# Optimization experiments

Hardware: AMD Instinct MI355X
Metric: run time of the kernel (lower is better)

Reference implementation:

```python
import jax, jax.numpy as jnp
import numpy as np

N_HEADS = 16

def setup_inputs() -> dict:
    key = jax.random.key(0)
    k1, k2, k3 = jax.random.split(key, 3)
    B, L, D = 2, 2048, 1024
    x = jax.random.normal(k1, (B, L, D), dtype=jnp.float32)
    w_qkv = jax.random.normal(k2, (D, 3 * D), dtype=jnp.float32) * (1.0 / np.sqrt(D))
    w_out = jax.random.normal(k3, (D, D), dtype=jnp.float32) * (1.0 / np.sqrt(D))
    return {"x": x, "w_qkv": w_qkv, "w_out": w_out}

def reference(x, w_qkv, w_out):
    B, L, D = x.shape
    H = N_HEADS
    dh = D // H
    qkv = x @ w_qkv                      # (B, L, 3D)
    q, k, v = jnp.split(qkv, 3, axis=-1)
    # (B, H, L, dh)
    q = q.reshape(B, L, H, dh).transpose(0, 2, 1, 3)
    k = k.reshape(B, L, H, dh).transpose(0, 2, 1, 3)
    v = v.reshape(B, L, H, dh).transpose(0, 2, 1, 3)
    scale = 1.0 / jnp.sqrt(jnp.asarray(dh, x.dtype))
    attn = jnp.einsum('bhqd,bhkd->bhqk', q, k) * scale   # (B, H, L, L)
    causal = jnp.tril(jnp.ones((L, L), dtype=bool))
    attn = jnp.where(causal[None, None], attn, -jnp.inf)
    attn = jax.nn.softmax(attn, axis=-1)
    out = jnp.einsum('bhqk,bhkd->bhqd', attn, v)         # (B, H, L, dh)
    out = out.transpose(0, 2, 1, 3).reshape(B, L, D)
    return out @ w_out
```

## Files before the change

### kernel.cpp

```cpp
#include <hip/hip_runtime.h>

typedef __attribute__((ext_vector_type(4))) float f32x4;
typedef __attribute__((ext_vector_type(16))) float f32x16;
typedef __attribute__((ext_vector_type(8))) __bf16 bf16x8;
typedef __attribute__((ext_vector_type(4))) __bf16 bf16x4;
typedef __attribute__((ext_vector_type(4))) unsigned u32x4;
typedef __attribute__((ext_vector_type(2))) unsigned u32x2;

static __device__ __forceinline__ f32x4 mfma16(bf16x8 a, bf16x8 b, f32x4 c) {
    return __builtin_amdgcn_mfma_f32_16x16x32_bf16(a, b, c, 0, 0, 0);
}
static __device__ __forceinline__ f32x16 mfma32(bf16x8 a, bf16x8 b, f32x16 c) {
    return __builtin_amdgcn_mfma_f32_32x32x16_bf16(a, b, c, 0, 0, 0);
}
static __device__ __forceinline__ unsigned pk_bf16(float a, float b) {
    unsigned lo = __builtin_bit_cast(unsigned short, (__bf16)a);
    unsigned hh = __builtin_bit_cast(unsigned short, (__bf16)b);
    return lo | (hh << 16);
}

#define QSCALE 0.18033688f

__global__ __launch_bounds__(256) void cvt_f32_bf16(const float* __restrict__ in,
                                                    __bf16* __restrict__ out, int n4) {
    int i = blockIdx.x * 256 + threadIdx.x;
    if (i < n4) {
        f32x4 v = ((const f32x4*)in)[i];
        bf16x4 o;
#pragma unroll
        for (int j = 0; j < 4; j++) o[j] = (__bf16)v[j];
        ((bf16x4*)out)[i] = o;
    }
}

__global__ __launch_bounds__(256) void transpose_bf16(const float* __restrict__ in,
                                                      __bf16* __restrict__ out,
                                                      int R, int C) {
    __shared__ float t[32][33];
    int bx = blockIdx.x * 32;
    int by = blockIdx.y * 32;
    int tx = threadIdx.x, ty = threadIdx.y;
#pragma unroll
    for (int k = 0; k < 32; k += 8)
        t[ty + k][tx] = in[(size_t)(by + ty + k) * C + bx + tx];
    __syncthreads();
#pragma unroll
    for (int k = 0; k < 32; k += 8)
        out[(size_t)(bx + ty + k) * R + by + tx] = (__bf16)t[tx][ty + k];
}

#define BM 128
#define BN 128
#define BKG 64

template <int MODE>
__global__ __launch_bounds__(256) void gemm_bt(const __bf16* __restrict__ A,
                                               const __bf16* __restrict__ Bt,
                                               int M, int N, int K,
                                               float* __restrict__ Cout,
                                               __bf16* __restrict__ Qf,
                                               __bf16* __restrict__ Kf,
                                               __bf16* __restrict__ Vf) {
    __shared__ __attribute__((aligned(16))) __bf16 As[BM * BKG];
    __shared__ __attribute__((aligned(16))) __bf16 Bs[BN * BKG];
    int tid = threadIdx.x;
    int wave = tid >> 6, lane = tid & 63;
    int lrow = lane & 15, lgrp = lane >> 4;
    int chunk = gridDim.x >> 3;
    int bid = blockIdx.x;
    int swz = (bid & 7) * chunk + (bid >> 3);
    int nbx = N >> 7;
    int m0 = (swz / nbx) * BM, n0 = (swz % nbx) * BN;
    int wm = (wave >> 1) * 64, wn = (wave & 1) * 64;

    f32x4 acc[4][4];
#pragma unroll
    for (int i = 0; i < 4; i++)
#pragma unroll
        for (int j = 0; j < 4; j++) acc[i][j] = (f32x4){0.f, 0.f, 0.f, 0.f};

    int srow = tid >> 3;
    int gch = (tid & 7) ^ (srow & 7);
    const __bf16* aSrc = A + (size_t)(m0 + srow) * K + gch * 8;
    const __bf16* bSrc = Bt + (size_t)(n0 + srow) * K + gch * 8;

    for (int k0 = 0; k0 < K; k0 += BKG) {
#pragma unroll
        for (int c = 0; c < 4; c++) {
            __builtin_amdgcn_global_load_lds(
                (const __attribute__((address_space(1))) void*)(aSrc + k0 + (size_t)c * 32 * K),
                (__attribute__((address_space(3))) void*)(As + (c * 256 + wave * 64) * 8),
                16, 0, 0);
        }
#pragma unroll
        for (int c = 0; c < 4; c++) {
            __builtin_amdgcn_global_load_lds(
                (const __attribute__((address_space(1))) void*)(bSrc + k0 + (size_t)c * 32 * K),
                (__attribute__((address_space(3))) void*)(Bs + (c * 256 + wave * 64) * 8),
                16, 0, 0);
        }
        __syncthreads();
#pragma unroll
        for (int kk = 0; kk < 2; kk++) {
            bf16x8 af[4], bfr[4];
#pragma unroll
            for (int mt = 0; mt < 4; mt++) {
                int row = wm + mt * 16 + lrow;
                int slot = row * 8 + ((4 * kk + lgrp) ^ (row & 7));
                af[mt] = *(const bf16x8*)(As + slot * 8);
            }
#pragma unroll
            for (int nt = 0; nt < 4; nt++) {
                int row = wn + nt * 16 + lrow;
                int slot = row * 8 + ((4 * kk + lgrp) ^ (row & 7));
                bfr[nt] = *(const bf16x8*)(Bs + slot * 8);
            }
#pragma unroll
            for (int mt = 0; mt < 4; mt++)
#pragma unroll
                for (int nt = 0; nt < 4; nt++)
                    acc[mt][nt] = mfma16(af[mt], bfr[nt], acc[mt][nt]);
        }
        __syncthreads();
    }

#pragma unroll
    for (int mt = 0; mt < 4; mt++) {
#pragma unroll
        for (int nt = 0; nt < 4; nt++) {
            int f0 = m0 + wm + mt * 16 + lgrp * 4;
            int t = n0 + wn + nt * 16 + lrow;
            if (MODE == 0) {
                *(f32x4*)(Cout + (size_t)t * M + f0) = acc[mt][nt];
            } else {
                int which = f0 >> 10, hn = f0 & 1023;
                int h = hn >> 6, d0 = hn & 63;
                int b = t >> 11, li = t & 2047;
                int bh = b * 16 + h, c = li >> 5, tl = li & 31;
                size_t bhbase = (size_t)bh * 131072;
                if (which == 2) {
                    int ks = tl >> 4, hv = (tl >> 3) & 1, jv = tl & 7;
                    size_t base =
                        bhbase + ((size_t)(c * 4 + ks * 2 + hv) * 64 + d0) * 8 + jv;
#pragma unroll
                    for (int r = 0; r < 4; r++)
                        Vf[base + (size_t)r * 8] = (__bf16)acc[mt][nt][r];
                } else {
                    int st = d0 >> 4, hv = (d0 >> 3) & 1, j0 = d0 & 7;
                    size_t idx =
                        bhbase + ((size_t)(c * 8 + st * 2 + hv) * 32 + tl) * 8 + j0;
                    bf16x4 pv;
                    if (which == 0) {
#pragma unroll
                        for (int r = 0; r < 4; r++)
                            pv[r] = (__bf16)(acc[mt][nt][r] * QSCALE);
                        *(bf16x4*)(Qf + idx) = pv;
                    } else {
#pragma unroll
                        for (int r = 0; r < 4; r++) pv[r] = (__bf16)acc[mt][nt][r];
                        *(bf16x4*)(Kf + idx) = pv;
                    }
                }
            }
        }
    }
}

template <bool MASKED>
static __device__ __forceinline__ void attn_chunk(
    int c, int ql, int hi, const __bf16* __restrict__ Kp,
    const __bf16* __restrict__ Vp, const bf16x8 (&qf)[4],
    f32x16& o0, f32x16& o1, float& ls) {
    const __bf16* kb = Kp + ((size_t)c * 8 + hi) * 256 + ql * 8;
    bf16x8 kf[4];
#pragma unroll
    for (int st = 0; st < 4; st++) kf[st] = *(const bf16x8*)(kb + st * 512);
    const __bf16* vb = Vp + ((size_t)c * 4 + hi) * 512 + ql * 8;
    bf16x8 v00 = *(const bf16x8*)(vb);
    bf16x8 v01 = *(const bf16x8*)(vb + 256);
    bf16x8 v10 = *(const bf16x8*)(vb + 1024);
    bf16x8 v11 = *(const bf16x8*)(vb + 1280);

    f32x16 sa;
#pragma unroll
    for (int r = 0; r < 16; r++) sa[r] = 0.f;
#pragma unroll
    for (int st = 0; st < 4; st++) sa = mfma32(kf[st], qf[st], sa);

    float p[16];
    float psum = 0.f;
#pragma unroll
    for (int r = 0; r < 16; r++) {
        float s = sa[r];
        if (MASKED) {
            int krel = (r & 3) + 8 * (r >> 2) + 4 * hi;
            if (krel > ql) s = -1e30f;
        }
        float pv = __builtin_amdgcn_exp2f(s);
        p[r] = pv;
        psum += pv;
    }
    u32x2 ps = __builtin_amdgcn_permlane32_swap(
        __builtin_bit_cast(unsigned, psum), __builtin_bit_cast(unsigned, psum),
        false, false);
    psum += __builtin_bit_cast(float, hi ? ps[0] : ps[1]);
    ls += psum;

    unsigned w[8];
#pragma unroll
    for (int i = 0; i < 8; i++) w[i] = pk_bf16(p[2 * i], p[2 * i + 1]);
    u32x2 r02 = __builtin_amdgcn_permlane32_swap(w[0], w[2], false, false);
    u32x2 r13 = __builtin_amdgcn_permlane32_swap(w[1], w[3], false, false);
    u32x2 r46 = __builtin_amdgcn_permlane32_swap(w[4], w[6], false, false);
    u32x2 r57 = __builtin_amdgcn_permlane32_swap(w[5], w[7], false, false);
    bf16x8 pa0 = __builtin_bit_cast(bf16x8, (u32x4){r02[0], r13[0], r02[1], r13[1]});
    bf16x8 pa1 = __builtin_bit_cast(bf16x8, (u32x4){r46[0], r57[0], r46[1], r57[1]});

    o0 = mfma32(pa0, v00, o0);
    o1 = mfma32(pa0, v01, o1);
    o0 = mfma32(pa1, v10, o0);
    o1 = mfma32(pa1, v11, o1);
}

__global__ __launch_bounds__(256) void attn_fwd5(const __bf16* __restrict__ Qf,
                                                 const __bf16* __restrict__ Kf,
                                                 const __bf16* __restrict__ Vf,
                                                 __bf16* __restrict__ Ob) {
    __shared__ float comb[3][64][33];
    int tid = threadIdx.x;
    int wave = tid >> 6, lane = tid & 63;
    int ql = lane & 31, hi = lane >> 5;
    int bid = blockIdx.x;
    int xcd = bid & 7, idx = bid >> 3;
    int bh = xcd * 4 + (idx >> 6);
    int strip = 63 - (idx & 63);
    int q0 = strip * 32;

    const __bf16* Qp = Qf + (size_t)bh * 131072;
    const __bf16* Kp = Kf + (size_t)bh * 131072;
    const __bf16* Vp = Vf + (size_t)bh * 131072;

    const __bf16* qb = Qp + ((size_t)strip * 8 + hi) * 256 + ql * 8;
    bf16x8 qf[4];
#pragma unroll
    for (int st = 0; st < 4; st++) qf[st] = *(const bf16x8*)(qb + st * 512);

    f32x16 o0, o1;
#pragma unroll
    for (int r = 0; r < 16; r++) { o0[r] = 0.f; o1[r] = 0.f; }
    float ls = 0.f;

    for (int c = wave; c < strip; c += 4)
        attn_chunk<false>(c, ql, hi, Kp, Vp, qf, o0, o1, ls);
    if ((strip & 3) == wave)
        attn_chunk<true>(strip, ql, hi, Kp, Vp, qf, o0, o1, ls);

    if (wave >= 1) {
        float* sl = &comb[wave - 1][lane][0];
#pragma unroll
        for (int r = 0; r < 16; r++) { sl[r] = o0[r]; sl[16 + r] = o1[r]; }
        sl[32] = ls;
    }
    __syncthreads();
    if (wave == 0) {
#pragma unroll
        for (int s = 0; s < 3; s++) {
            const float* sl = &comb[s][lane][0];
#pragma unroll
            for (int r = 0; r < 16; r++) { o0[r] += sl[r]; o1[r] += sl[16 + r]; }
            ls += sl[32];
        }
        float inv = 1.0f / ls;
        int b = bh >> 4, h = bh & 15;
#pragma unroll
        for (int r = 0; r < 16; r++) {
            int crow = (r & 3) + 8 * (r >> 2) + 4 * hi;
            float ibc = __shfl(inv, crow);
            size_t base = ((size_t)(b * 2048 + q0 + crow)) * 1024 + h * 64;
            Ob[base + ql] = (__bf16)(o0[r] * ibc);
            Ob[base + 32 + ql] = (__bf16)(o1[r] * ibc);
        }
    }
}

extern "C" void kernel_launch(void* const* d_in, const int* in_sizes, int n_in,
                              void* d_out, int out_size, void* d_ws, size_t ws_size,
                              hipStream_t stream) {
    const float* x = (const float*)d_in[0];
    const float* w_qkv = (const float*)d_in[1];
    const float* w_out = (const float*)d_in[2];
    float* out = (float*)d_out;

    char* ws = (char*)d_ws;
    __bf16* xb    = (__bf16*)(ws);
    __bf16* wqkvT = (__bf16*)(ws + (size_t)(8  << 20));
    __bf16* woutT = (__bf16*)(ws + (size_t)(14 << 20));
    __bf16* Qf    = (__bf16*)(ws + (size_t)(16 << 20));
    __bf16* Kf    = (__bf16*)(ws + (size_t)(24 << 20));
    __bf16* Vf    = (__bf16*)(ws + (size_t)(32 << 20));
    __bf16* Ob    = (__bf16*)(ws + (size_t)(40 << 20));

    cvt_f32_bf16<<<4096, 256, 0, stream>>>(x, xb, 4096 * 1024 / 4);
    transpose_bf16<<<dim3(3072 / 32, 1024 / 32), dim3(32, 8), 0, stream>>>(w_qkv, wqkvT, 1024, 3072);
    transpose_bf16<<<dim3(1024 / 32, 1024 / 32), dim3(32, 8), 0, stream>>>(w_out, woutT, 1024, 1024);
    gemm_bt<1><<<768, 256, 0, stream>>>(
        wqkvT, xb, 3072, 4096, 1024, nullptr, Qf, Kf, Vf);
    attn_fwd5<<<2048, 256, 0, stream>>>(Qf, Kf, Vf, Ob);
    gemm_bt<0><<<256, 256, 0, stream>>>(
        woutT, Ob, 1024, 4096, 1024, out, nullptr, nullptr, nullptr);
}
```

Measured before the change: 110.3 us.

## Share K/V tiles across waves via LDS double-buffering and fuse prep kernels

The attention kernel now gives each wave its own 32-row query strip inside a 128-row tile. All waves share K/V chunks that are staged into LDS with global_load_lds and double-buffered, which replaces per-wave global K/V loads and the cross-wave reduction through shared memory. This is meant to cut global memory traffic for K/V and drop the final combine step. The trade-off is a block-wide barrier every chunk, and waves with short causal ranges sit idle while still taking part in staging. Separately, the bf16 conversion and the two weight transposes are merged into one launch to save launch overhead.

```diff
diff --git a/kernel.cpp b/kernel.cpp
--- a/kernel.cpp
+++ b/kernel.cpp
@@ -21,25 +21,36 @@
 
 #define QSCALE 0.18033688f
 
-__global__ __launch_bounds__(256) void cvt_f32_bf16(const float* __restrict__ in,
-                                                    __bf16* __restrict__ out, int n4) {
-    int i = blockIdx.x * 256 + threadIdx.x;
-    if (i < n4) {
-        f32x4 v = ((const f32x4*)in)[i];
+__global__ __launch_bounds__(256) void prep_all(const float* __restrict__ x,
+                                                __bf16* __restrict__ xb,
+                                                const float* __restrict__ wq,
+                                                __bf16* __restrict__ wqT,
+                                                const float* __restrict__ wo,
+                                                __bf16* __restrict__ woT) {
+    __shared__ float t[32][33];
+    int bid = blockIdx.x, tid = threadIdx.x;
+    if (bid < 4096) {
+        int i = bid * 256 + tid;
+        f32x4 v = ((const f32x4*)x)[i];
         bf16x4 o;
 #pragma unroll
         for (int j = 0; j < 4; j++) o[j] = (__bf16)v[j];
-        ((bf16x4*)out)[i] = o;
-    }
-}
-
-__global__ __launch_bounds__(256) void transpose_bf16(const float* __restrict__ in,
-                                                      __bf16* __restrict__ out,
-                                                      int R, int C) {
-    __shared__ float t[32][33];
-    int bx = blockIdx.x * 32;
-    int by = blockIdx.y * 32;
-    int tx = threadIdx.x, ty = threadIdx.y;
+        ((bf16x4*)xb)[i] = o;
+        return;
+    }
+    const float* in;
+    __bf16* out;
+    int R, C, bx, by;
+    if (bid < 4096 + 3072) {
+        int b2 = bid - 4096;
+        in = wq; out = wqT; R = 1024; C = 3072;
+        bx = (b2 % 96) * 32; by = (b2 / 96) * 32;
+    } else {
+        int b2 = bid - 7168;
+        in = wo; out = woT; R = 1024; C = 1024;
+        bx = (b2 % 32) * 32; by = (b2 / 32) * 32;
+    }
+    int tx = tid & 31, ty = tid >> 5;
 #pragma unroll
     for (int k = 0; k < 32; k += 8)
         t[ty + k][tx] = in[(size_t)(by + ty + k) * C + bx + tx];
@@ -166,81 +177,27 @@
     }
 }
 
-template <bool MASKED>
-static __device__ __forceinline__ void attn_chunk(
-    int c, int ql, int hi, const __bf16* __restrict__ Kp,
-    const __bf16* __restrict__ Vp, const bf16x8 (&qf)[4],
-    f32x16& o0, f32x16& o1, float& ls) {
-    const __bf16* kb = Kp + ((size_t)c * 8 + hi) * 256 + ql * 8;
-    bf16x8 kf[4];
-#pragma unroll
-    for (int st = 0; st < 4; st++) kf[st] = *(const bf16x8*)(kb + st * 512);
-    const __bf16* vb = Vp + ((size_t)c * 4 + hi) * 512 + ql * 8;
-    bf16x8 v00 = *(const bf16x8*)(vb);
-    bf16x8 v01 = *(const bf16x8*)(vb + 256);
-    bf16x8 v10 = *(const bf16x8*)(vb + 1024);
-    bf16x8 v11 = *(const bf16x8*)(vb + 1280);
-
-    f32x16 sa;
-#pragma unroll
-    for (int r = 0; r < 16; r++) sa[r] = 0.f;
-#pragma unroll
-    for (int st = 0; st < 4; st++) sa = mfma32(kf[st], qf[st], sa);
-
-    float p[16];
-    float psum = 0.f;
-#pragma unroll
-    for (int r = 0; r < 16; r++) {
-        float s = sa[r];
-        if (MASKED) {
-            int krel = (r & 3) + 8 * (r >> 2) + 4 * hi;
-            if (krel > ql) s = -1e30f;
-        }
-        float pv = __builtin_amdgcn_exp2f(s);
-        p[r] = pv;
-        psum += pv;
-    }
-    u32x2 ps = __builtin_amdgcn_permlane32_swap(
-        __builtin_bit_cast(unsigned, psum), __builtin_bit_cast(unsigned, psum),
-        false, false);
-    psum += __builtin_bit_cast(float, hi ? ps[0] : ps[1]);
-    ls += psum;
-
-    unsigned w[8];
-#pragma unroll
-    for (int i = 0; i < 8; i++) w[i] = pk_bf16(p[2 * i], p[2 * i + 1]);
-    u32x2 r02 = __builtin_amdgcn_permlane32_swap(w[0], w[2], false, false);
-    u32x2 r13 = __builtin_amdgcn_permlane32_swap(w[1], w[3], false, false);
-    u32x2 r46 = __builtin_amdgcn_permlane32_swap(w[4], w[6], false, false);
-    u32x2 r57 = __builtin_amdgcn_permlane32_swap(w[5], w[7], false, false);
-    bf16x8 pa0 = __builtin_bit_cast(bf16x8, (u32x4){r02[0], r13[0], r02[1], r13[1]});
-    bf16x8 pa1 = __builtin_bit_cast(bf16x8, (u32x4){r46[0], r57[0], r46[1], r57[1]});
-
-    o0 = mfma32(pa0, v00, o0);
-    o1 = mfma32(pa0, v01, o1);
-    o0 = mfma32(pa1, v10, o0);
-    o1 = mfma32(pa1, v11, o1);
-}
-
-__global__ __launch_bounds__(256) void attn_fwd5(const __bf16* __restrict__ Qf,
+__global__ __launch_bounds__(256) void attn_fwd9(const __bf16* __restrict__ Qf,
                                                  const __bf16* __restrict__ Kf,
                                                  const __bf16* __restrict__ Vf,
                                                  __bf16* __restrict__ Ob) {
-    __shared__ float comb[3][64][33];
+    __shared__ __attribute__((aligned(16))) __bf16 kv[2][4096];
     int tid = threadIdx.x;
     int wave = tid >> 6, lane = tid & 63;
     int ql = lane & 31, hi = lane >> 5;
     int bid = blockIdx.x;
     int xcd = bid & 7, idx = bid >> 3;
-    int bh = xcd * 4 + (idx >> 6);
-    int strip = 63 - (idx & 63);
-    int q0 = strip * 32;
+    int bh = xcd * 4 + (idx >> 4);
+    int tile = 15 - (idx & 15);
+    int S = tile * 4 + wave;
+    int q0 = S * 32;
+    int cmax = tile * 4 + 3;
 
     const __bf16* Qp = Qf + (size_t)bh * 131072;
     const __bf16* Kp = Kf + (size_t)bh * 131072;
     const __bf16* Vp = Vf + (size_t)bh * 131072;
 
-    const __bf16* qb = Qp + ((size_t)strip * 8 + hi) * 256 + ql * 8;
+    const __bf16* qb = Qp + ((size_t)S * 8 + hi) * 256 + ql * 8;
     bf16x8 qf[4];
 #pragma unroll
     for (int st = 0; st < 4; st++) qf[st] = *(const bf16x8*)(qb + st * 512);
@@ -250,36 +207,88 @@
     for (int r = 0; r < 16; r++) { o0[r] = 0.f; o1[r] = 0.f; }
     float ls = 0.f;
 
-    for (int c = wave; c < strip; c += 4)
-        attn_chunk<false>(c, ql, hi, Kp, Vp, qf, o0, o1, ls);
-    if ((strip & 3) == wave)
-        attn_chunk<true>(strip, ql, hi, Kp, Vp, qf, o0, o1, ls);
-
-    if (wave >= 1) {
-        float* sl = &comb[wave - 1][lane][0];
-#pragma unroll
-        for (int r = 0; r < 16; r++) { sl[r] = o0[r]; sl[16 + r] = o1[r]; }
-        sl[32] = ls;
-    }
+    auto STAGE = [&](int c, int b) {
+        const __bf16* sK = Kp + (size_t)c * 2048 + wave * 512 + lane * 8;
+        const __bf16* sV = Vp + (size_t)c * 2048 + wave * 512 + lane * 8;
+        __builtin_amdgcn_global_load_lds(
+            (const __attribute__((address_space(1))) void*)sK,
+            (__attribute__((address_space(3))) void*)(&kv[b][wave * 512]), 16, 0, 0);
+        __builtin_amdgcn_global_load_lds(
+            (const __attribute__((address_space(1))) void*)sV,
+            (__attribute__((address_space(3))) void*)(&kv[b][2048 + wave * 512]), 16, 0, 0);
+    };
+
+    auto COMPUTE = [&](int b, bool masked) {
+        const __bf16* kb = &kv[b][hi * 256 + ql * 8];
+        bf16x8 kf[4];
+#pragma unroll
+        for (int st = 0; st < 4; st++) kf[st] = *(const bf16x8*)(kb + st * 512);
+        const __bf16* vb = &kv[b][2048 + hi * 512 + ql * 8];
+        bf16x8 v00 = *(const bf16x8*)(vb);
+        bf16x8 v01 = *(const bf16x8*)(vb + 256);
+        bf16x8 v10 = *(const bf16x8*)(vb + 1024);
+        bf16x8 v11 = *(const bf16x8*)(vb + 1280);
+
+        f32x16 sa;
+#pragma unroll
+        for (int r = 0; r < 16; r++) sa[r] = 0.f;
+#pragma unroll
+        for (int st = 0; st < 4; st++) sa = mfma32(kf[st], qf[st], sa);
+
+        float p[16];
+        float psum = 0.f;
+#pragma unroll
+        for (int r = 0; r < 16; r++) {
+            float s = sa[r];
+            if (masked) {
+                int krel = (r & 3) + 8 * (r >> 2) + 4 * hi;
+                if (krel > ql) s = -1e30f;
+            }
+            float pv = __builtin_amdgcn_exp2f(s);
+            p[r] = pv;
+            psum += pv;
+        }
+        u32x2 ps = __builtin_amdgcn_permlane32_swap(
+            __builtin_bit_cast(unsigned, psum), __builtin_bit_cast(unsigned, psum),
+            false, false);
+        psum += __builtin_bit_cast(float, hi ? ps[0] : ps[1]);
+        ls += psum;
+
+        unsigned w[8];
+#pragma unroll
+        for (int i = 0; i < 8; i++) w[i] = pk_bf16(p[2 * i], p[2 * i + 1]);
+        u32x2 r02 = __builtin_amdgcn_permlane32_swap(w[0], w[2], false, false);
+        u32x2 r13 = __builtin_amdgcn_permlane32_swap(w[1], w[3], false, false);
+        u32x2 r46 = __builtin_amdgcn_permlane32_swap(w[4], w[6], false, false);
+        u32x2 r57 = __builtin_amdgcn_permlane32_swap(w[5], w[7], false, false);
+        bf16x8 pa0 = __builtin_bit_cast(bf16x8, (u32x4){r02[0], r13[0], r02[1], r13[1]});
+        bf16x8 pa1 = __builtin_bit_cast(bf16x8, (u32x4){r46[0], r57[0], r46[1], r57[1]});
+
+        o0 = mfma32(pa0, v00, o0);
+        o1 = mfma32(pa0, v01, o1);
+        o0 = mfma32(pa1, v10, o0);
+        o1 = mfma32(pa1, v11, o1);
+    };
+
+    STAGE(0, 0);
     __syncthreads();
-    if (wave == 0) {
-#pragma unroll
-        for (int s = 0; s < 3; s++) {
-            const float* sl = &comb[s][lane][0];
-#pragma unroll
-            for (int r = 0; r < 16; r++) { o0[r] += sl[r]; o1[r] += sl[16 + r]; }
-            ls += sl[32];
-        }
-        float inv = 1.0f / ls;
-        int b = bh >> 4, h = bh & 15;
-#pragma unroll
-        for (int r = 0; r < 16; r++) {
-            int crow = (r & 3) + 8 * (r >> 2) + 4 * hi;
-            float ibc = __shfl(inv, crow);
-            size_t base = ((size_t)(b * 2048 + q0 + crow)) * 1024 + h * 64;
-            Ob[base + ql] = (__bf16)(o0[r] * ibc);
-            Ob[base + 32 + ql] = (__bf16)(o1[r] * ibc);
-        }
+    for (int c = 0; c <= cmax; c++) {
+        int b = c & 1;
+        if (c < cmax) STAGE(c + 1, b ^ 1);
+        if (c < S) COMPUTE(b, false);
+        else if (c == S) COMPUTE(b, true);
+        __syncthreads();
+    }
+
+    float inv = 1.0f / ls;
+    int b_ = bh >> 4, h = bh & 15;
+#pragma unroll
+    for (int r = 0; r < 16; r++) {
+        int crow = (r & 3) + 8 * (r >> 2) + 4 * hi;
+        float ibc = __shfl(inv, crow);
+        size_t base = ((size_t)(b_ * 2048 + q0 + crow)) * 1024 + h * 64;
+        Ob[base + ql] = (__bf16)(o0[r] * ibc);
+        Ob[base + 32 + ql] = (__bf16)(o1[r] * ibc);
     }
 }
 
@@ -300,12 +309,10 @@
     __bf16* Vf    = (__bf16*)(ws + (size_t)(32 << 20));
     __bf16* Ob    = (__bf16*)(ws + (size_t)(40 << 20));
 
-    cvt_f32_bf16<<<4096, 256, 0, stream>>>(x, xb, 4096 * 1024 / 4);
-    transpose_bf16<<<dim3(3072 / 32, 1024 / 32), dim3(32, 8), 0, stream>>>(w_qkv, wqkvT, 1024, 3072);
-    transpose_bf16<<<dim3(1024 / 32, 1024 / 32), dim3(32, 8), 0, stream>>>(w_out, woutT, 1024, 1024);
+    prep_all<<<8192, 256, 0, stream>>>(x, xb, w_qkv, wqkvT, w_out, woutT);
     gemm_bt<1><<<768, 256, 0, stream>>>(
         wqkvT, xb, 3072, 4096, 1024, nullptr, Qf, Kf, Vf);
-    attn_fwd5<<<2048, 256, 0, stream>>>(Qf, Kf, Vf, Ob);
+    attn_fwd9<<<512, 256, 0, stream>>>(Qf, Kf, Vf, Ob);
     gemm_bt<0><<<256, 256, 0, stream>>>(
         woutT, Ob, 1024, 4096, 1024, out, nullptr, nullptr, nullptr);
 }
```

Measured after the change: 123.2 us. +11.6%, slower.

## Merge prep kernels and compute softmax row sums via MFMA with ones

Applied to the files above, without the earlier changes.

The three preprocessing launches (x conversion and two weight transposes) are merged into one kernel that dispatches on block index, removing two launch gaps. In attention, the softmax denominator is now accumulated by extra MFMAs against a vector of ones instead of a scalar sum plus a cross-lane permlane swap. The per-row reciprocal is then available in every lane and needs no shuffle, and launch bounds now request 4 blocks per CU. This adds two MFMAs per chunk and a third 16-register accumulator, and it enlarges the shared-memory combine buffer.

```diff
diff --git a/kernel.cpp b/kernel.cpp
--- a/kernel.cpp
+++ b/kernel.cpp
@@ -21,25 +21,36 @@
 
 #define QSCALE 0.18033688f
 
-__global__ __launch_bounds__(256) void cvt_f32_bf16(const float* __restrict__ in,
-                                                    __bf16* __restrict__ out, int n4) {
-    int i = blockIdx.x * 256 + threadIdx.x;
-    if (i < n4) {
-        f32x4 v = ((const f32x4*)in)[i];
+__global__ __launch_bounds__(256) void prep_all(const float* __restrict__ x,
+                                                __bf16* __restrict__ xb,
+                                                const float* __restrict__ wq,
+                                                __bf16* __restrict__ wqT,
+                                                const float* __restrict__ wo,
+                                                __bf16* __restrict__ woT) {
+    __shared__ float t[32][33];
+    int bid = blockIdx.x, tid = threadIdx.x;
+    if (bid < 4096) {
+        int i = bid * 256 + tid;
+        f32x4 v = ((const f32x4*)x)[i];
         bf16x4 o;
 #pragma unroll
         for (int j = 0; j < 4; j++) o[j] = (__bf16)v[j];
-        ((bf16x4*)out)[i] = o;
-    }
-}
-
-__global__ __launch_bounds__(256) void transpose_bf16(const float* __restrict__ in,
-                                                      __bf16* __restrict__ out,
-                                                      int R, int C) {
-    __shared__ float t[32][33];
-    int bx = blockIdx.x * 32;
-    int by = blockIdx.y * 32;
-    int tx = threadIdx.x, ty = threadIdx.y;
+        ((bf16x4*)xb)[i] = o;
+        return;
+    }
+    const float* in;
+    __bf16* out;
+    int R, C, bx, by;
+    if (bid < 4096 + 3072) {
+        int b2 = bid - 4096;
+        in = wq; out = wqT; R = 1024; C = 3072;
+        bx = (b2 % 96) * 32; by = (b2 / 96) * 32;
+    } else {
+        int b2 = bid - 7168;
+        in = wo; out = woT; R = 1024; C = 1024;
+        bx = (b2 % 32) * 32; by = (b2 / 32) * 32;
+    }
+    int tx = tid & 31, ty = tid >> 5;
 #pragma unroll
     for (int k = 0; k < 32; k += 8)
         t[ty + k][tx] = in[(size_t)(by + ty + k) * C + bx + tx];
@@ -169,8 +180,8 @@
 template <bool MASKED>
 static __device__ __forceinline__ void attn_chunk(
     int c, int ql, int hi, const __bf16* __restrict__ Kp,
-    const __bf16* __restrict__ Vp, const bf16x8 (&qf)[4],
-    f32x16& o0, f32x16& o1, float& ls) {
+    const __bf16* __restrict__ Vp, const bf16x8 (&qf)[4], bf16x8 ones,
+    f32x16& o0, f32x16& o1, f32x16& lsa) {
     const __bf16* kb = Kp + ((size_t)c * 8 + hi) * 256 + ql * 8;
     bf16x8 kf[4];
 #pragma unroll
@@ -188,7 +199,6 @@
     for (int st = 0; st < 4; st++) sa = mfma32(kf[st], qf[st], sa);
 
     float p[16];
-    float psum = 0.f;
 #pragma unroll
     for (int r = 0; r < 16; r++) {
         float s = sa[r];
@@ -196,15 +206,8 @@
             int krel = (r & 3) + 8 * (r >> 2) + 4 * hi;
             if (krel > ql) s = -1e30f;
         }
-        float pv = __builtin_amdgcn_exp2f(s);
-        p[r] = pv;
-        psum += pv;
-    }
-    u32x2 ps = __builtin_amdgcn_permlane32_swap(
-        __builtin_bit_cast(unsigned, psum), __builtin_bit_cast(unsigned, psum),
-        false, false);
-    psum += __builtin_bit_cast(float, hi ? ps[0] : ps[1]);
-    ls += psum;
+        p[r] = __builtin_amdgcn_exp2f(s);
+    }
 
     unsigned w[8];
 #pragma unroll
@@ -218,15 +221,17 @@
 
     o0 = mfma32(pa0, v00, o0);
     o1 = mfma32(pa0, v01, o1);
+    lsa = mfma32(pa0, ones, lsa);
     o0 = mfma32(pa1, v10, o0);
     o1 = mfma32(pa1, v11, o1);
-}
-
-__global__ __launch_bounds__(256) void attn_fwd5(const __bf16* __restrict__ Qf,
-                                                 const __bf16* __restrict__ Kf,
-                                                 const __bf16* __restrict__ Vf,
-                                                 __bf16* __restrict__ Ob) {
-    __shared__ float comb[3][64][33];
+    lsa = mfma32(pa1, ones, lsa);
+}
+
+__global__ __launch_bounds__(256, 4) void attn_fwd10(const __bf16* __restrict__ Qf,
+                                                     const __bf16* __restrict__ Kf,
+                                                     const __bf16* __restrict__ Vf,
+                                                     __bf16* __restrict__ Ob) {
+    __shared__ float comb[3][64][49];
     int tid = threadIdx.x;
     int wave = tid >> 6, lane = tid & 63;
     int ql = lane & 31, hi = lane >> 5;
@@ -245,21 +250,25 @@
 #pragma unroll
     for (int st = 0; st < 4; st++) qf[st] = *(const bf16x8*)(qb + st * 512);
 
-    f32x16 o0, o1;
-#pragma unroll
-    for (int r = 0; r < 16; r++) { o0[r] = 0.f; o1[r] = 0.f; }
-    float ls = 0.f;
+    bf16x8 ones;
+#pragma unroll
+    for (int j = 0; j < 8; j++) ones[j] = (__bf16)1.0f;
+
+    f32x16 o0, o1, lsa;
+#pragma unroll
+    for (int r = 0; r < 16; r++) { o0[r] = 0.f; o1[r] = 0.f; lsa[r] = 0.f; }
 
     for (int c = wave; c < strip; c += 4)
-        attn_chunk<false>(c, ql, hi, Kp, Vp, qf, o0, o1, ls);
+        attn_chunk<false>(c, ql, hi, Kp, Vp, qf, ones, o0, o1, lsa);
     if ((strip & 3) == wave)
-        attn_chunk<true>(strip, ql, hi, Kp, Vp, qf, o0, o1, ls);
+        attn_chunk<true>(strip, ql, hi, Kp, Vp, qf, ones, o0, o1, lsa);
 
     if (wave >= 1) {
         float* sl = &comb[wave - 1][lane][0];
 #pragma unroll
-        for (int r = 0; r < 16; r++) { sl[r] = o0[r]; sl[16 + r] = o1[r]; }
-        sl[32] = ls;
+        for (int r = 0; r < 16; r++) {
+            sl[r] = o0[r]; sl[16 + r] = o1[r]; sl[32 + r] = lsa[r];
+        }
     }
     __syncthreads();
     if (wave == 0) {
@@ -267,18 +276,19 @@
         for (int s = 0; s < 3; s++) {
             const float* sl = &comb[s][lane][0];
 #pragma unroll
-            for (int r = 0; r < 16; r++) { o0[r] += sl[r]; o1[r] += sl[16 + r]; }
-            ls += sl[32];
-        }
-        float inv = 1.0f / ls;
+            for (int r = 0; r < 16; r++) {
+                o0[r] += sl[r]; o1[r] += sl[16 + r]; lsa[r] += sl[32 + r];
+            }
+        }
         int b = bh >> 4, h = bh & 15;
 #pragma unroll
         for (int r = 0; r < 16; r++) {
             int crow = (r & 3) + 8 * (r >> 2) + 4 * hi;
-            float ibc = __shfl(inv, crow);
+            float inv;
+            asm("v_rcp_f32 %0, %1" : "=v"(inv) : "v"(lsa[r]));
             size_t base = ((size_t)(b * 2048 + q0 + crow)) * 1024 + h * 64;
-            Ob[base + ql] = (__bf16)(o0[r] * ibc);
-            Ob[base + 32 + ql] = (__bf16)(o1[r] * ibc);
+            Ob[base + ql] = (__bf16)(o0[r] * inv);
+            Ob[base + 32 + ql] = (__bf16)(o1[r] * inv);
         }
     }
 }
@@ -300,12 +310,10 @@
     __bf16* Vf    = (__bf16*)(ws + (size_t)(32 << 20));
     __bf16* Ob    = (__bf16*)(ws + (size_t)(40 << 20));
 
-    cvt_f32_bf16<<<4096, 256, 0, stream>>>(x, xb, 4096 * 1024 / 4);
-    transpose_bf16<<<dim3(3072 / 32, 1024 / 32), dim3(32, 8), 0, stream>>>(w_qkv, wqkvT, 1024, 3072);
-    transpose_bf16<<<dim3(1024 / 32, 1024 / 32), dim3(32, 8), 0, stream>>>(w_out, woutT, 1024, 1024);
+    prep_all<<<8192, 256, 0, stream>>>(x, xb, w_qkv, wqkvT, w_out, woutT);
     gemm_bt<1><<<768, 256, 0, stream>>>(
         wqkvT, xb, 3072, 4096, 1024, nullptr, Qf, Kf, Vf);
-    attn_fwd5<<<2048, 256, 0, stream>>>(Qf, Kf, Vf, Ob);
+    attn_fwd10<<<2048, 256, 0, stream>>>(Qf, Kf, Vf, Ob);
     gemm_bt<0><<<256, 256, 0, stream>>>(
         woutT, Ob, 1024, 4096, 1024, out, nullptr, nullptr, nullptr);
 }
```

Measured after the change: 103.4 us. 6.3% less time.
